# Optimization experiments

Hardware: AMD Instinct MI355X
Metric: run time of the kernel (lower is better)

## Reference

```python
import jax, jax.numpy as jnp
import numpy as np

EPS = 1e-5

def layernorm(x, g, b):
    mu = jnp.mean(x, axis=-1, keepdims=True)
    var = jnp.mean(jnp.square(x - mu), axis=-1, keepdims=True)
    return (x - mu) * jax.lax.rsqrt(var + EPS) * g + b

def rope(x):
    # x: [B, H, S, hd]; faithful to source: theta = 10000**(-2*pos/hd), pos in {0,2,4,...}
    S, hd = x.shape[-2], x.shape[-1]
    pos2 = jnp.arange(0, hd, 2, dtype=jnp.float32)
    theta = jnp.power(10000.0, -2.0 * pos2 / hd)          # [hd/2]
    ang = jnp.arange(S, dtype=jnp.float32)[:, None] * theta  # [S, hd/2]
    cos, sin = jnp.cos(ang), jnp.sin(ang)                  # broadcast over B,H
    xr = x.reshape(*x.shape[:-1], hd // 2, 2)
    x0, x1 = xr[..., 0], xr[..., 1]
    out = jnp.stack([x0 * cos - x1 * sin, x1 * cos + x0 * sin], axis=-1)
    return out.reshape(x.shape)

def setup_inputs() -> dict:
    key = jax.random.key(0)
    ks = jax.random.split(key, 8)
    B, S, D, H = 2, 2048, 1024, 16
    hd = D // H
    s_in = 1.0 / np.sqrt(D)
    s_h = 1.0 / np.sqrt(2 * D)
    return {
        "x": jax.random.normal(ks[0], (B, S, D), jnp.float32),
        "ln1_g": jnp.ones((D,), jnp.float32),
        "ln1_b": jnp.zeros((D,), jnp.float32),
        "Wq": jax.random.normal(ks[1], (H, D, hd), jnp.float32) * s_in,
        "Wk": jax.random.normal(ks[2], (H, D, hd), jnp.float32) * s_in,
        "Wv": jax.random.normal(ks[3], (H, D, hd), jnp.float32) * s_in,
        "Wo": jax.random.normal(ks[4], (D, D), jnp.float32) * s_in,
        "ln2_g": jnp.ones((D,), jnp.float32),
        "ln2_b": jnp.zeros((D,), jnp.float32),
        "W1": jax.random.normal(ks[5], (D, 2 * D), jnp.float32) * s_in,
        "W2": jax.random.normal(ks[6], (D, 2 * D), jnp.float32) * s_in,
        "W3": jax.random.normal(ks[7], (2 * D, D), jnp.float32) * s_h,
    }

def reference(x, ln1_g, ln1_b, Wq, Wk, Wv, Wo, ln2_g, ln2_b, W1, W2, W3):
    B, S, D = x.shape
    # --- attention sublayer ---
    h = layernorm(x, ln1_g, ln1_b)
    q = jnp.einsum("bsd,hdk->bhsk", h, Wq)
    k = jnp.einsum("bsd,hdk->bhsk", h, Wk)
    v = jnp.einsum("bsd,hdk->bhsk", h, Wv)
    q, k = rope(q), rope(k)
    hd = q.shape[-1]
    scores = jnp.einsum("bhqk,bhsk->bhqs", q, k) * (hd ** -0.5)  # [B,H,S,S]
    causal = jnp.tril(jnp.ones((S, S), bool))
    scores = jnp.where(causal, scores, jnp.float32(-jnp.inf))
    attn = jax.nn.softmax(scores, axis=-1)
    o = jnp.einsum("bhqs,bhsk->bhqk", attn, v)                   # [B,H,S,hd]
    o = o.transpose(0, 2, 1, 3).reshape(B, S, D)                 # concat heads
    x = x + o @ Wo
    # --- SwiGLU FFN sublayer ---
    h2 = layernorm(x, ln2_g, ln2_b)
    u = h2 @ W1
    ffn = (u * jax.nn.sigmoid(u)) * (h2 @ W2)
    return x + ffn @ W3
```

## Files before the change

### kernel.cpp

```cpp
#include <hip/hip_runtime.h>
#include <hip/hip_bf16.h>

using bf16 = __hip_bfloat16;
typedef __attribute__((ext_vector_type(8))) short bf16x8;
typedef __attribute__((ext_vector_type(4))) float f32x4;


__device__ inline float toF(float x) { return x; }
__device__ inline float toF(bf16 x) { return __bfloat162float(x); }

__device__ __forceinline__ void unpack8(uint4 u, float* f) {
    f[0] = __uint_as_float(u.x << 16); f[1] = __uint_as_float(u.x & 0xffff0000u);
    f[2] = __uint_as_float(u.y << 16); f[3] = __uint_as_float(u.y & 0xffff0000u);
    f[4] = __uint_as_float(u.z << 16); f[5] = __uint_as_float(u.z & 0xffff0000u);
    f[6] = __uint_as_float(u.w << 16); f[7] = __uint_as_float(u.w & 0xffff0000u);
}

__device__ __forceinline__ uint4 packbf8(const float* f) {
    union { unsigned short u[8]; uint4 v; } r;
#pragma unroll
    for (int i = 0; i < 8; i++) {
        bf16 b = __float2bfloat16(f[i]);
        r.u[i] = *(unsigned short*)&b;
    }
    return r.v;
}

__device__ __forceinline__ unsigned pack2(float lo, float hi) {
    bf16 a = __float2bfloat16(lo), b = __float2bfloat16(hi);
    return ((unsigned)*(unsigned short*)&b << 16) | (unsigned)*(unsigned short*)&a;
}

__device__ __forceinline__ void gl_lds16(const void* g, void* l) {
    __builtin_amdgcn_global_load_lds(
        (__attribute__((address_space(1))) void*)g,
        (__attribute__((address_space(3))) void*)l, 16, 0, 0);
}

template <typename Tx>
__device__ __forceinline__ void ln_body(
    const Tx* __restrict__ x, const float* __restrict__ g,
    const float* __restrict__ b, bf16* __restrict__ out, int row,
    float* s1, float* s2)
{
    const int D = 1024;
    int tid = threadIdx.x;
    const Tx* xr = x + (size_t)row * D;

    float vals[4];
    float sum = 0.f, sumsq = 0.f;
#pragma unroll
    for (int i = 0; i < 4; i++) {
        float v = toF(xr[tid + i * 256]);
        vals[i] = v; sum += v; sumsq += v * v;
    }
#pragma unroll
    for (int off = 32; off > 0; off >>= 1) {
        sum += __shfl_xor(sum, off);
        sumsq += __shfl_xor(sumsq, off);
    }
    int wave = tid >> 6, lane = tid & 63;
    if (lane == 0) { s1[wave] = sum; s2[wave] = sumsq; }
    __syncthreads();
    sum = s1[0] + s1[1] + s1[2] + s1[3];
    sumsq = s2[0] + s2[1] + s2[2] + s2[3];

    float mu = sum * (1.f / D);
    float var = sumsq * (1.f / D) - mu * mu;
    float rstd = rsqrtf(var + 1e-5f);

    bf16* orow = out + (size_t)row * D;
#pragma unroll
    for (int i = 0; i < 4; i++) {
        int c = tid + i * 256;
        orow[c] = __float2bfloat16((vals[i] - mu) * rstd * g[c] + b[c]);
    }
}

__global__ __launch_bounds__(256) void prep1_kernel(
    const float* __restrict__ x, const float* __restrict__ g,
    const float* __restrict__ b, bf16* __restrict__ h,
    const float* __restrict__ Wq, const float* __restrict__ Wk,
    const float* __restrict__ Wv, const float* __restrict__ Wo,
    bf16* __restrict__ wt)
{
    __shared__ float t[32][33];
    __shared__ float s1[4], s2[4];
    int bx = blockIdx.x;
    if (bx < 2048) {
        ln_body<float>(x, g, b, h, bx, s1, s2);
        return;
    }
    int zz = bx - 2048;
    int z = zz >> 6, rem = zz & 63;
    int yy = rem >> 1, xx = rem & 1;
    const float* ip; int ldi;
    if (z < 48) {
        const float* s = (z < 16) ? Wq : (z < 32) ? Wk : Wv;
        ip = s + (size_t)(z & 15) * 65536; ldi = 64;
    } else {
        ip = Wo + (size_t)(z - 48) * 64; ldi = 1024;
    }
    bf16* op = wt + ((size_t)z << 16);
    int c0 = xx * 32, r0 = yy * 32;
    int tx = threadIdx.x & 31, ty = threadIdx.x >> 5;
#pragma unroll
    for (int i = 0; i < 4; i++)
        t[ty + 8 * i][tx] = ip[(size_t)(r0 + ty + 8 * i) * ldi + c0 + tx];
    __syncthreads();
#pragma unroll
    for (int i = 0; i < 4; i++)
        op[(size_t)(c0 + ty + 8 * i) * 1024 + r0 + tx] = __float2bfloat16(t[tx][ty + 8 * i]);
}

__global__ __launch_bounds__(256) void prep2_kernel(
    const bf16* __restrict__ x2, const float* __restrict__ g,
    const float* __restrict__ b, bf16* __restrict__ h2,
    const float* __restrict__ W1, const float* __restrict__ W2,
    bf16* __restrict__ wt)
{
    __shared__ float t[32][33];
    __shared__ float s1[4], s2[4];
    int bx = blockIdx.x;
    if (bx < 2048) {
        ln_body<bf16>(x2, g, b, h2, bx, s1, s2);
        return;
    }
    int zz = bx - 2048;
    int xx = zz & 63, yy = (zz >> 6) & 31, z = zz >> 11;
    const float* ip = z ? W2 : W1;
    bf16* op = wt + ((size_t)z << 21);
    int c0 = xx * 32, r0 = yy * 32;
    int tx = threadIdx.x & 31, ty = threadIdx.x >> 5;
#pragma unroll
    for (int i = 0; i < 4; i++)
        t[ty + 8 * i][tx] = ip[(size_t)(r0 + ty + 8 * i) * 2048 + c0 + tx];
    __syncthreads();
#pragma unroll
    for (int i = 0; i < 4; i++)
        op[(size_t)(c0 + ty + 8 * i) * 1024 + r0 + tx] = __float2bfloat16(t[tx][ty + 8 * i]);
}

__global__ __launch_bounds__(256) void tconv_kernel(
    const float* __restrict__ in, bf16* __restrict__ out, int R, int C)
{
    __shared__ float t[32][33];
    const float* ip = in;
    bf16* op = out;
    int c0 = blockIdx.x * 32, r0 = blockIdx.y * 32;
    int tx = threadIdx.x & 31, ty = threadIdx.x >> 5;
#pragma unroll
    for (int i = 0; i < 4; i++)
        t[ty + 8 * i][tx] = ip[(size_t)(r0 + ty + 8 * i) * C + c0 + tx];
    __syncthreads();
#pragma unroll
    for (int i = 0; i < 4; i++)
        op[(size_t)(c0 + ty + 8 * i) * R + r0 + tx] = __float2bfloat16(t[tx][ty + 8 * i]);
}

template <int MODE>
__global__ __launch_bounds__(256) void mfma_gemm(
    const bf16* __restrict__ A, const bf16* __restrict__ BT0,
    void* __restrict__ Cv, const void* __restrict__ resv,
    int M, int N, int K)
{
    constexpr int NB = (MODE == 5) ? 3 : 2;
    __shared__ bf16 smem[2][NB][64 * 64];
    int tid = threadIdx.x, lane = tid & 63, w = tid >> 6;
    int wm = w >> 1, wn = w & 1;
    int m0 = blockIdx.y * 64, n0 = blockIdx.x * 64;

    const bf16* BT = BT0;
    bf16* Cq = nullptr; int rope = 0;
    if (MODE == 1) {
        int z = blockIdx.z;
        BT = BT0 + ((size_t)z << 20);
        Cq = (bf16*)Cv + ((size_t)z << 21);
        rope = (z < 2);
    }

    int lrow = lane >> 3;
    int lcb  = (lane & 7) ^ lrow;
    const bf16* Ag  = A  + (size_t)(m0 + w * 8 + lrow) * K + lcb * 8;
    const bf16* Bg0 = BT + (size_t)(n0 + w * 8 + lrow) * K + lcb * 8;
    const bf16* B2g = (MODE == 5)
        ? (const bf16*)resv + (size_t)(n0 + w * 8 + lrow) * K + lcb * 8
        : nullptr;
    unsigned sbase = (unsigned)__builtin_amdgcn_readfirstlane(w * 8 * 128);
    char* smc = (char*)smem;

    f32x4 acc[2][2], acc2[2][2];
#pragma unroll
    for (int i = 0; i < 2; i++)
#pragma unroll
        for (int j = 0; j < 2; j++) {
            acc[i][j] = (f32x4){0.f, 0.f, 0.f, 0.f};
            if (MODE == 5) acc2[i][j] = (f32x4){0.f, 0.f, 0.f, 0.f};
        }

    int cidx = lane & 15, quad = lane >> 4;

    auto STAGE = [&](int buf, int k0) {
        char* p = smc + (size_t)buf * (NB * 8192) + sbase;
        gl_lds16(Ag + k0,                   p);
        gl_lds16(Ag + (size_t)32 * K + k0,  p + 4096);
        gl_lds16(Bg0 + k0,                  p + 8192);
        gl_lds16(Bg0 + (size_t)32 * K + k0, p + 12288);
        if (MODE == 5) {
            gl_lds16(B2g + k0,                  p + 16384);
            gl_lds16(B2g + (size_t)32 * K + k0, p + 20480);
        }
    };

    STAGE(0, 0);
    __syncthreads();
    int cur = 0;
    for (int k0 = 0; k0 < K; k0 += 64) {
        if (k0 + 64 < K) STAGE(cur ^ 1, k0 + 64);
        const bf16* Ab = (const bf16*)(smc + (size_t)cur * (NB * 8192));
        const bf16* Bb = Ab + 4096;
        const bf16* B2b = Ab + 8192;
#pragma unroll
        for (int kk = 0; kk < 2; kk++) {
            int pb = (kk * 4 + quad) ^ (cidx & 7);
            bf16x8 af[2], bfr[2], b2f[2];
#pragma unroll
            for (int i = 0; i < 2; i++)
                af[i] = *(const bf16x8*)&Ab[(wm * 32 + i * 16 + cidx) * 64 + pb * 8];
#pragma unroll
            for (int j = 0; j < 2; j++)
                bfr[j] = *(const bf16x8*)&Bb[(wn * 32 + j * 16 + cidx) * 64 + pb * 8];
            if (MODE == 5) {
#pragma unroll
                for (int j = 0; j < 2; j++)
                    b2f[j] = *(const bf16x8*)&B2b[(wn * 32 + j * 16 + cidx) * 64 + pb * 8];
            }
            __builtin_amdgcn_s_setprio(1);
#pragma unroll
            for (int i = 0; i < 2; i++)
#pragma unroll
                for (int j = 0; j < 2; j++) {
                    acc[i][j] = __builtin_amdgcn_mfma_f32_16x16x32_bf16(af[i], bfr[j], acc[i][j], 0, 0, 0);
                    if (MODE == 5)
                        acc2[i][j] = __builtin_amdgcn_mfma_f32_16x16x32_bf16(af[i], b2f[j], acc2[i][j], 0, 0, 0);
                }
            __builtin_amdgcn_s_setprio(0);
        }
        __syncthreads();
        cur ^= 1;
    }

    int rbase = quad * 4;
#pragma unroll
    for (int i = 0; i < 2; i++) {
#pragma unroll
        for (int j = 0; j < 2; j++) {
            int row0 = m0 + wm * 32 + i * 16 + rbase;
            int col = n0 + wn * 32 + j * 16 + cidx;
            if (MODE == 1 && !rope) {
                int h_ = col >> 6, d = col & 63;
                uint2 t;
                t.x = pack2(acc[i][j][0], acc[i][j][1]);
                t.y = pack2(acc[i][j][2], acc[i][j][3]);
                *(uint2*)&Cq[(size_t)h_ * 131072 + (size_t)d * 2048 + row0] = t;
                continue;
            }
#pragma unroll
            for (int r = 0; r < 4; r++) {
                int row = row0 + r;
                float v = acc[i][j][r];
                size_t idx = (size_t)row * N + col;
                if (MODE == 1) {
                    int h_ = col >> 6, kk = col & 63;
                    float other = __shfl_xor(v, 1);
                    float p = (float)(kk >> 1);
                    float theta = __expf(p * -0.5756462732485114f);
                    float ang = (float)row * theta;
                    float c, sn; __sincosf(ang, &sn, &c);
                    float outv = (kk & 1) ? (v * c + other * sn) : (v * c - other * sn);
                    Cq[((size_t)h_ * 2048 + row) * 64 + kk] = __float2bfloat16(outv);
                } else if (MODE == 2) {
                    v += ((const float*)resv)[idx];
                    ((bf16*)Cv)[idx] = __float2bfloat16(v);
                } else if (MODE == 5) {
                    float g2 = acc2[i][j][r];
                    float sg = 1.f / (1.f + __expf(-v));
                    ((bf16*)Cv)[idx] = __float2bfloat16(v * sg * g2);
                } else {
                    v += __bfloat162float(((const bf16*)resv)[idx]);
                    ((float*)Cv)[idx] = v;
                }
            }
        }
    }
}

__global__ __launch_bounds__(256) void attn_kernel(
    const bf16* __restrict__ q, const bf16* __restrict__ k,
    const bf16* __restrict__ vt, bf16* __restrict__ o)
{
    const int S = 2048;
    __shared__ bf16 Ks[64 * 64];
    __shared__ bf16 Vs[64 * 64];
    __shared__ __align__(16) char QPbuf[64 * 72 * 2];

    int h = blockIdx.y;
    int qt = (h & 8) ? (int)blockIdx.x : 31 - (int)blockIdx.x;
    int tid = threadIdx.x, lane = tid & 63, w = tid >> 6;
    int quad = lane >> 4, cidx = lane & 15;
    int m0 = qt * 64;

    const bf16* qb = q + ((size_t)h * S + m0) * 64;
    const bf16* kb = k + (size_t)h * S * 64;
    const bf16* vtb = vt + (size_t)h * 64 * S;

    int srow = tid >> 2;
    int sg = (tid & 3) * 16;

    bf16 (*Qs)[72] = (bf16 (*)[72])QPbuf;
    {
        const uint4* src = (const uint4*)(qb + (size_t)srow * 64 + sg);
        uint4 u0 = src[0], u1 = src[1];
        float f[16]; unpack8(u0, f); unpack8(u1, f + 8);
#pragma unroll
        for (int i = 0; i < 16; i++) f[i] *= 0.125f * 1.44269504f;
        *(uint4*)&Qs[srow][sg] = packbf8(f);
        *(uint4*)&Qs[srow][sg + 8] = packbf8(f + 8);
    }
    bf16x8 bQ0 = *(const bf16x8*)&Qs[w * 16 + cidx][quad * 8];
    bf16x8 bQ1 = *(const bf16x8*)&Qs[w * 16 + cidx][32 + quad * 8];

    unsigned* Pst = (unsigned*)QPbuf + w * 576;

    int cb0 = (tid & 3) * 2;
    int sw0 = ((cb0)     ^ (srow & 7)) * 8;
    int sw1 = ((cb0 + 1) ^ (srow & 7)) * 8;
    int pb0 = ((quad)     ^ (cidx & 7)) * 8;
    int pb1 = ((4 + quad) ^ (cidx & 7)) * 8;

    float m_i = -INFINITY, l_i = 0.f;
    f32x4 Oc[4];
#pragma unroll
    for (int i = 0; i < 4; i++) Oc[i] = (f32x4){0.f, 0.f, 0.f, 0.f};

    uint4 ka0, ka1, va0, va1;
    {
        const uint4* ksrc = (const uint4*)(kb + (size_t)srow * 64 + sg);
        ka0 = ksrc[0]; ka1 = ksrc[1];
        const uint4* vsrc = (const uint4*)(vtb + (size_t)srow * S + sg);
        va0 = vsrc[0]; va1 = vsrc[1];
    }

    for (int kt = 0; kt <= qt; kt++) {
        __syncthreads();
        *(uint4*)&Ks[srow * 64 + sw0] = ka0;
        *(uint4*)&Ks[srow * 64 + sw1] = ka1;
        *(uint4*)&Vs[srow * 64 + sw0] = va0;
        *(uint4*)&Vs[srow * 64 + sw1] = va1;
        __syncthreads();
        if (kt < qt) {
            const uint4* kn = (const uint4*)(kb + (size_t)((kt + 1) * 64 + srow) * 64 + sg);
            ka0 = kn[0]; ka1 = kn[1];
            const uint4* vn = (const uint4*)(vtb + (size_t)srow * S + (kt + 1) * 64 + sg);
            va0 = vn[0]; va1 = vn[1];
        }

        f32x4 sc[4];
#pragma unroll
        for (int i = 0; i < 4; i++) {
            bf16x8 aK0 = *(const bf16x8*)&Ks[(i * 16 + cidx) * 64 + pb0];
            bf16x8 aK1 = *(const bf16x8*)&Ks[(i * 16 + cidx) * 64 + pb1];
            f32x4 z = (f32x4){0.f, 0.f, 0.f, 0.f};
            __builtin_amdgcn_s_setprio(1);
            z = __builtin_amdgcn_mfma_f32_16x16x32_bf16(aK0, bQ0, z, 0, 0, 0);
            z = __builtin_amdgcn_mfma_f32_16x16x32_bf16(aK1, bQ1, z, 0, 0, 0);
            __builtin_amdgcn_s_setprio(0);
            sc[i] = z;
        }

        if (kt == qt) {
#pragma unroll
            for (int i = 0; i < 4; i++)
#pragma unroll
                for (int r = 0; r < 4; r++)
                    if (i * 16 + quad * 4 + r > w * 16 + cidx) sc[i][r] = -INFINITY;
        }

        float l0 = fmaxf(fmaxf(sc[0][0], sc[0][1]), fmaxf(sc[0][2], sc[0][3]));
        float l1 = fmaxf(fmaxf(sc[1][0], sc[1][1]), fmaxf(sc[1][2], sc[1][3]));
        float l2 = fmaxf(fmaxf(sc[2][0], sc[2][1]), fmaxf(sc[2][2], sc[2][3]));
        float l3 = fmaxf(fmaxf(sc[3][0], sc[3][1]), fmaxf(sc[3][2], sc[3][3]));
        float lmax = fmaxf(fmaxf(l0, l1), fmaxf(l2, l3));

        if (!__all(lmax <= m_i + 8.f)) {
            float pmax = fmaxf(lmax, __shfl_xor(lmax, 16));
            pmax = fmaxf(pmax, __shfl_xor(pmax, 32));
            float mnew = fmaxf(m_i, pmax);
            float alpha = __builtin_amdgcn_exp2f(m_i - mnew);
            l_i *= alpha;
#pragma unroll
            for (int i = 0; i < 4; i++) {
                Oc[i][0] *= alpha; Oc[i][1] *= alpha;
                Oc[i][2] *= alpha; Oc[i][3] *= alpha;
            }
            m_i = mnew;
        }

        float rs = 0.f;
#pragma unroll
        for (int i = 0; i < 4; i++)
#pragma unroll
            for (int r = 0; r < 4; r++) {
                sc[i][r] = __builtin_amdgcn_exp2f(sc[i][r] - m_i);
                rs += sc[i][r];
            }
        l_i += rs;

#pragma unroll
        for (int i = 0; i < 4; i++) {
            uint2 t;
            t.x = pack2(sc[i][0], sc[i][1]);
            t.y = pack2(sc[i][2], sc[i][3]);
            *(uint2*)&Pst[cidx * 36 + 8 * i + 2 * quad] = t;
        }
        bf16x8 bP0 = *(const bf16x8*)&Pst[cidx * 36 + 4 * quad];
        bf16x8 bP1 = *(const bf16x8*)&Pst[cidx * 36 + 16 + 4 * quad];

#pragma unroll
        for (int i = 0; i < 4; i++) {
            bf16x8 aV0 = *(const bf16x8*)&Vs[(i * 16 + cidx) * 64 + pb0];
            bf16x8 aV1 = *(const bf16x8*)&Vs[(i * 16 + cidx) * 64 + pb1];
            __builtin_amdgcn_s_setprio(1);
            Oc[i] = __builtin_amdgcn_mfma_f32_16x16x32_bf16(aV0, bP0, Oc[i], 0, 0, 0);
            Oc[i] = __builtin_amdgcn_mfma_f32_16x16x32_bf16(aV1, bP1, Oc[i], 0, 0, 0);
            __builtin_amdgcn_s_setprio(0);
        }
    }

    float lr = l_i;
    lr += __shfl_xor(lr, 16);
    lr += __shfl_xor(lr, 32);
    float inv = 1.f / lr;
#pragma unroll
    for (int i = 0; i < 4; i++) {
        uint2 t;
        t.x = pack2(Oc[i][0] * inv, Oc[i][1] * inv);
        t.y = pack2(Oc[i][2] * inv, Oc[i][3] * inv);
        *(uint2*)&Pst[cidx * 36 + 8 * i + 2 * quad] = t;
    }
    int r2 = lane >> 2, g2 = (lane & 3) * 8;
    uint4 o0 = *(const uint4*)&Pst[r2 * 36 + g2];
    uint4 o1 = *(const uint4*)&Pst[r2 * 36 + g2 + 4];
    bf16* orow = o + (size_t)(m0 + w * 16 + r2) * 1024 + h * 64;
    *(uint4*)(orow + g2 * 2) = o0;
    *(uint4*)(orow + g2 * 2 + 8) = o1;
}

extern "C" void kernel_launch(void* const* d_in, const int* in_sizes, int n_in,
                              void* d_out, int out_size, void* d_ws, size_t ws_size,
                              hipStream_t stream)
{
    const int S = 2048, D = 1024;

    const float* x    = (const float*)d_in[0];
    const float* ln1g = (const float*)d_in[1];
    const float* ln1b = (const float*)d_in[2];
    const float* Wq   = (const float*)d_in[3];
    const float* Wk   = (const float*)d_in[4];
    const float* Wv   = (const float*)d_in[5];
    const float* Wo   = (const float*)d_in[6];
    const float* ln2g = (const float*)d_in[7];
    const float* ln2b = (const float*)d_in[8];
    const float* W1   = (const float*)d_in[9];
    const float* W2   = (const float*)d_in[10];
    const float* W3   = (const float*)d_in[11];
    float* out = (float*)d_out;

    const size_t NR = (size_t)S * D;
    bf16* r0 = (bf16*)d_ws;
    bf16* r1 = r0 + NR;
    bf16* r2 = r1 + NR;
    bf16* r3 = r2 + NR;
    const size_t M1 = 1u << 20;

    for (int b = 0; b < 2; b++) {
        const float* xb = x + (size_t)b * S * D;
        float* ob = out + (size_t)b * S * D;
        bf16* pb = (bf16*)ob;

        prep1_kernel<<<6144, 256, 0, stream>>>(xb, ln1g, ln1b, r3,
                                               Wq, Wk, Wv, Wo, pb);

        mfma_gemm<1><<<dim3(16, 32, 3), 256, 0, stream>>>(r3, pb, r0, nullptr, S, 1024, 1024);

        attn_kernel<<<dim3(32, 16), 256, 0, stream>>>(r0, r1, r2, pb);

        mfma_gemm<2><<<dim3(16, 32, 1), 256, 0, stream>>>(pb, pb + 3 * M1, r3, xb, S, 1024, 1024);

        prep2_kernel<<<6144, 256, 0, stream>>>(r3, ln2g, ln2b, r0, W1, W2, pb);

        mfma_gemm<5><<<dim3(32, 32, 1), 256, 0, stream>>>(r0, pb, r1, pb + 2 * M1, S, 2048, 1024);

        tconv_kernel<<<dim3(32, 64), 256, 0, stream>>>(W3, r0, 2048, 1024);

        mfma_gemm<4><<<dim3(16, 32, 1), 256, 0, stream>>>(r1, r0, ob, r3, S, 1024, 2048);
    }
}
```

Baseline: 366.6 us.

## Batch both sequences into shared launches for LN, QKV, attention and Wo stages

```diff
diff --git a/kernel.cpp b/kernel.cpp
--- a/kernel.cpp
+++ b/kernel.cpp
@@ -79,34 +79,29 @@
 
 __global__ __launch_bounds__(256) void prep1_kernel(
     const float* __restrict__ x, const float* __restrict__ g,
-    const float* __restrict__ b, bf16* __restrict__ h,
+    const float* __restrict__ b, bf16* __restrict__ h0, bf16* __restrict__ h1,
     const float* __restrict__ Wq, const float* __restrict__ Wk,
-    const float* __restrict__ Wv, const float* __restrict__ Wo,
-    bf16* __restrict__ wt)
+    const float* __restrict__ Wv, bf16* __restrict__ wt)
 {
     __shared__ float t[32][33];
     __shared__ float s1[4], s2[4];
     int bx = blockIdx.x;
-    if (bx < 2048) {
-        ln_body<float>(x, g, b, h, bx, s1, s2);
+    if (bx < 4096) {
+        int bb = bx >> 11, row = bx & 2047;
+        ln_body<float>(x + ((size_t)bb << 21), g, b, bb ? h1 : h0, row, s1, s2);
         return;
     }
-    int zz = bx - 2048;
+    int zz = bx - 4096;
     int z = zz >> 6, rem = zz & 63;
     int yy = rem >> 1, xx = rem & 1;
-    const float* ip; int ldi;
-    if (z < 48) {
-        const float* s = (z < 16) ? Wq : (z < 32) ? Wk : Wv;
-        ip = s + (size_t)(z & 15) * 65536; ldi = 64;
-    } else {
-        ip = Wo + (size_t)(z - 48) * 64; ldi = 1024;
-    }
+    const float* s = (z < 16) ? Wq : (z < 32) ? Wk : Wv;
+    const float* ip = s + (size_t)(z & 15) * 65536;
     bf16* op = wt + ((size_t)z << 16);
     int c0 = xx * 32, r0 = yy * 32;
     int tx = threadIdx.x & 31, ty = threadIdx.x >> 5;
 #pragma unroll
     for (int i = 0; i < 4; i++)
-        t[ty + 8 * i][tx] = ip[(size_t)(r0 + ty + 8 * i) * ldi + c0 + tx];
+        t[ty + 8 * i][tx] = ip[(size_t)(r0 + ty + 8 * i) * 64 + c0 + tx];
     __syncthreads();
 #pragma unroll
     for (int i = 0; i < 4; i++)
@@ -145,23 +140,40 @@
     const float* __restrict__ in, bf16* __restrict__ out, int R, int C)
 {
     __shared__ float t[32][33];
-    const float* ip = in;
-    bf16* op = out;
     int c0 = blockIdx.x * 32, r0 = blockIdx.y * 32;
     int tx = threadIdx.x & 31, ty = threadIdx.x >> 5;
 #pragma unroll
     for (int i = 0; i < 4; i++)
-        t[ty + 8 * i][tx] = ip[(size_t)(r0 + ty + 8 * i) * C + c0 + tx];
+        t[ty + 8 * i][tx] = in[(size_t)(r0 + ty + 8 * i) * C + c0 + tx];
     __syncthreads();
 #pragma unroll
     for (int i = 0; i < 4; i++)
-        op[(size_t)(c0 + ty + 8 * i) * R + r0 + tx] = __float2bfloat16(t[tx][ty + 8 * i]);
+        out[(size_t)(c0 + ty + 8 * i) * R + r0 + tx] = __float2bfloat16(t[tx][ty + 8 * i]);
+}
+
+__global__ __launch_bounds__(256) void tconv_wo_kernel(
+    const float* __restrict__ Wo, bf16* __restrict__ out)
+{
+    __shared__ float t[32][33];
+    int z = blockIdx.z;
+    const float* ip = Wo + (size_t)z * 64;
+    bf16* op = out + ((size_t)z << 16);
+    int c0 = blockIdx.x * 32, r0 = blockIdx.y * 32;
+    int tx = threadIdx.x & 31, ty = threadIdx.x >> 5;
+#pragma unroll
+    for (int i = 0; i < 4; i++)
+        t[ty + 8 * i][tx] = ip[(size_t)(r0 + ty + 8 * i) * 1024 + c0 + tx];
+    __syncthreads();
+#pragma unroll
+    for (int i = 0; i < 4; i++)
+        op[(size_t)(c0 + ty + 8 * i) * 1024 + r0 + tx] = __float2bfloat16(t[tx][ty + 8 * i]);
 }
 
 template <int MODE>
 __global__ __launch_bounds__(256) void mfma_gemm(
     const bf16* __restrict__ A, const bf16* __restrict__ BT0,
     void* __restrict__ Cv, const void* __restrict__ resv,
+    const void* __restrict__ p5, void* __restrict__ p6,
     int M, int N, int K)
 {
     constexpr int NB = (MODE == 5) ? 3 : 2;
@@ -170,18 +182,27 @@
     int wm = w >> 1, wn = w & 1;
     int m0 = blockIdx.y * 64, n0 = blockIdx.x * 64;
 
+    const bf16* Ap = A;
     const bf16* BT = BT0;
-    bf16* Cq = nullptr; int rope = 0;
+    bf16* Cq = nullptr;
+    const float* resF = (const float*)resv;
+    void* Cdst = Cv;
     if (MODE == 1) {
         int z = blockIdx.z;
-        BT = BT0 + ((size_t)z << 20);
-        Cq = (bf16*)Cv + ((size_t)z << 21);
-        rope = (z < 2);
+        if (z >> 1) Ap = (const bf16*)resv;
+        BT = BT0 + ((size_t)(z & 1) << 20);
+        Cq = (bf16*)((z >> 1) ? p6 : Cv) + ((size_t)(z & 1) << 21);
+    }
+    if (MODE == 6) Cq = (bf16*)Cv;
+    if (MODE == 2) {
+        int z = blockIdx.z;
+        if (z) { Ap = (const bf16*)p5; Cdst = p6; }
+        resF = (const float*)resv + ((size_t)z << 21);
     }
 
     int lrow = lane >> 3;
     int lcb  = (lane & 7) ^ lrow;
-    const bf16* Ag  = A  + (size_t)(m0 + w * 8 + lrow) * K + lcb * 8;
+    const bf16* Ag  = Ap + (size_t)(m0 + w * 8 + lrow) * K + lcb * 8;
     const bf16* Bg0 = BT + (size_t)(n0 + w * 8 + lrow) * K + lcb * 8;
     const bf16* B2g = (MODE == 5)
         ? (const bf16*)resv + (size_t)(n0 + w * 8 + lrow) * K + lcb * 8
@@ -257,7 +278,7 @@
         for (int j = 0; j < 2; j++) {
             int row0 = m0 + wm * 32 + i * 16 + rbase;
             int col = n0 + wn * 32 + j * 16 + cidx;
-            if (MODE == 1 && !rope) {
+            if (MODE == 6) {
                 int h_ = col >> 6, d = col & 63;
                 uint2 t;
                 t.x = pack2(acc[i][j][0], acc[i][j][1]);
@@ -280,8 +301,8 @@
                     float outv = (kk & 1) ? (v * c + other * sn) : (v * c - other * sn);
                     Cq[((size_t)h_ * 2048 + row) * 64 + kk] = __float2bfloat16(outv);
                 } else if (MODE == 2) {
-                    v += ((const float*)resv)[idx];
-                    ((bf16*)Cv)[idx] = __float2bfloat16(v);
+                    v += resF[idx];
+                    ((bf16*)Cdst)[idx] = __float2bfloat16(v);
                 } else if (MODE == 5) {
                     float g2 = acc2[i][j][r];
                     float sg = 1.f / (1.f + __expf(-v));
@@ -296,13 +317,21 @@
 }
 
 __global__ __launch_bounds__(256) void attn_kernel(
-    const bf16* __restrict__ q, const bf16* __restrict__ k,
-    const bf16* __restrict__ vt, bf16* __restrict__ o)
+    const bf16* __restrict__ q0, const bf16* __restrict__ k0,
+    const bf16* __restrict__ vt0, bf16* __restrict__ o0,
+    const bf16* __restrict__ q1, const bf16* __restrict__ k1,
+    const bf16* __restrict__ vt1, bf16* __restrict__ o1)
 {
     const int S = 2048;
     __shared__ bf16 Ks[64 * 64];
     __shared__ bf16 Vs[64 * 64];
     __shared__ __align__(16) char QPbuf[64 * 72 * 2];
+
+    int zb = blockIdx.z;
+    const bf16* q = zb ? q1 : q0;
+    const bf16* k = zb ? k1 : k0;
+    const bf16* vt = zb ? vt1 : vt0;
+    bf16* o = zb ? o1 : o0;
 
     int h = blockIdx.y;
     int qt = (h & 8) ? (int)blockIdx.x : 31 - (int)blockIdx.x;
@@ -449,18 +478,18 @@
         *(uint2*)&Pst[cidx * 36 + 8 * i + 2 * quad] = t;
     }
     int r2 = lane >> 2, g2 = (lane & 3) * 8;
-    uint4 o0 = *(const uint4*)&Pst[r2 * 36 + g2];
-    uint4 o1 = *(const uint4*)&Pst[r2 * 36 + g2 + 4];
+    uint4 o0v = *(const uint4*)&Pst[r2 * 36 + g2];
+    uint4 o1v = *(const uint4*)&Pst[r2 * 36 + g2 + 4];
     bf16* orow = o + (size_t)(m0 + w * 16 + r2) * 1024 + h * 64;
-    *(uint4*)(orow + g2 * 2) = o0;
-    *(uint4*)(orow + g2 * 2 + 8) = o1;
+    *(uint4*)(orow + g2 * 2) = o0v;
+    *(uint4*)(orow + g2 * 2 + 8) = o1v;
 }
 
 extern "C" void kernel_launch(void* const* d_in, const int* in_sizes, int n_in,
                               void* d_out, int out_size, void* d_ws, size_t ws_size,
                               hipStream_t stream)
 {
-    const int S = 2048, D = 1024;
+    const int S = 2048;
 
     const float* x    = (const float*)d_in[0];
     const float* ln1g = (const float*)d_in[1];
@@ -476,33 +505,53 @@
     const float* W3   = (const float*)d_in[11];
     float* out = (float*)d_out;
 
-    const size_t NR = (size_t)S * D;
+    const size_t M2 = 1u << 21;
     bf16* r0 = (bf16*)d_ws;
-    bf16* r1 = r0 + NR;
-    bf16* r2 = r1 + NR;
-    bf16* r3 = r2 + NR;
-    const size_t M1 = 1u << 20;
-
-    for (int b = 0; b < 2; b++) {
-        const float* xb = x + (size_t)b * S * D;
-        float* ob = out + (size_t)b * S * D;
-        bf16* pb = (bf16*)ob;
-
-        prep1_kernel<<<6144, 256, 0, stream>>>(xb, ln1g, ln1b, r3,
-                                               Wq, Wk, Wv, Wo, pb);
-
-        mfma_gemm<1><<<dim3(16, 32, 3), 256, 0, stream>>>(r3, pb, r0, nullptr, S, 1024, 1024);
-
-        attn_kernel<<<dim3(32, 16), 256, 0, stream>>>(r0, r1, r2, pb);
-
-        mfma_gemm<2><<<dim3(16, 32, 1), 256, 0, stream>>>(pb, pb + 3 * M1, r3, xb, S, 1024, 1024);
-
-        prep2_kernel<<<6144, 256, 0, stream>>>(r3, ln2g, ln2b, r0, W1, W2, pb);
-
-        mfma_gemm<5><<<dim3(32, 32, 1), 256, 0, stream>>>(r0, pb, r1, pb + 2 * M1, S, 2048, 1024);
-
-        tconv_kernel<<<dim3(32, 64), 256, 0, stream>>>(W3, r0, 2048, 1024);
-
-        mfma_gemm<4><<<dim3(16, 32, 1), 256, 0, stream>>>(r1, r0, ob, r3, S, 1024, 2048);
-    }
-}
+    bf16* r1 = r0 + M2;
+    bf16* r2 = r1 + M2;
+    bf16* r3 = r2 + M2;
+    bf16* pb0 = (bf16*)out;
+    bf16* pb1 = pb0 + 2 * M2;
+    float* out0 = out;
+    float* out1 = out + (1u << 21);
+
+    prep1_kernel<<<7168, 256, 0, stream>>>(x, ln1g, ln1b, r0, r1,
+                                           Wq, Wk, Wv, pb0);
+
+    mfma_gemm<1><<<dim3(16, 32, 4), 256, 0, stream>>>(
+        r0, pb0, r2, r1, nullptr, pb1, S, 1024, 1024);
+
+    mfma_gemm<6><<<dim3(16, 32, 1), 256, 0, stream>>>(
+        r0, pb0 + M2, pb0, nullptr, nullptr, nullptr, S, 1024, 1024);
+
+    mfma_gemm<6><<<dim3(16, 32, 1), 256, 0, stream>>>(
+        r1, pb0 + M2, r0, nullptr, nullptr, nullptr, S, 1024, 1024);
+
+    attn_kernel<<<dim3(32, 16, 2), 256, 0, stream>>>(
+        r2, r3, pb0, r1, pb1, pb1 + M2, r0, pb0 + M2);
+
+    tconv_wo_kernel<<<dim3(2, 32, 16), 256, 0, stream>>>(Wo, r2);
+
+    mfma_gemm<2><<<dim3(16, 32, 2), 256, 0, stream>>>(
+        r1, r2, r3, x, pb0 + M2, r0, S, 1024, 1024);
+
+    prep2_kernel<<<6144, 256, 0, stream>>>(r3, ln2g, ln2b, pb1, W1, W2, pb0);
+
+    mfma_gemm<5><<<dim3(32, 32, 1), 256, 0, stream>>>(
+        pb1, pb0, r1, pb0 + M2, nullptr, nullptr, S, 2048, 1024);
+
+    tconv_kernel<<<dim3(32, 64), 256, 0, stream>>>(W3, pb1 + M2, 2048, 1024);
+
+    mfma_gemm<4><<<dim3(16, 32, 1), 256, 0, stream>>>(
+        r1, pb1 + M2, out0, r3, nullptr, nullptr, S, 1024, 2048);
+
+    prep2_kernel<<<6144, 256, 0, stream>>>(r0, ln2g, ln2b, r3, W1, W2, pb1);
+
+    mfma_gemm<5><<<dim3(32, 32, 1), 256, 0, stream>>>(
+        r3, pb1, r1, pb1 + M2, nullptr, nullptr, S, 2048, 1024);
+
+    tconv_kernel<<<dim3(32, 64), 256, 0, stream>>>(W3, r3, 2048, 1024);
+
+    mfma_gemm<4><<<dim3(16, 32, 1), 256, 0, stream>>>(
+        r1, r3, out1, r0, nullptr, nullptr, S, 1024, 2048);
+}
```

Measured after the change: 327.0 us. -10.8%, faster.
